# Optimization experiments

Hardware: AMD Instinct MI355X
Metric: run time of the kernel (lower is better)

## Reference

```python
import jax, jax.numpy as jnp
import numpy as np

C_Z = 128
H = 4
D = C_Z // H          # head_dim = 32
BASE = 2 * D // 2     # base_feature_dim = feature_map_multiplier*head_dim//2 = 32
BSZ, S = 1, 256
EPS_LN = 1e-5


def _lin_params(key, fan_in, fan_out):
    kw, kb = jax.random.split(key)
    bound = 1.0 / np.sqrt(fan_in)
    w = jax.random.uniform(kw, (fan_out, fan_in), jnp.float32, -bound, bound)
    b = jax.random.uniform(kb, (fan_out,), jnp.float32, -bound, bound)
    return w, b


def setup_inputs() -> dict:
    key = jax.random.key(0)
    ks = jax.random.split(key, 9)
    z = jax.random.normal(ks[0], (BSZ, S, S, C_Z), jnp.float32)
    pair_mask = jax.random.randint(ks[1], (BSZ, S, S), 0, 2, jnp.int32)
    q_w, q_b = _lin_params(ks[2], C_Z, C_Z)
    k_w, k_b = _lin_params(ks[3], C_Z, C_Z)
    v_w, v_b = _lin_params(ks[4], C_Z, C_Z)
    qf_w, qf_b = _lin_params(ks[5], D, BASE)
    kf_w, kf_b = _lin_params(ks[6], D, BASE)
    g_w, g_b = _lin_params(ks[7], C_Z, C_Z)
    o_w, o_b = _lin_params(ks[8], C_Z, C_Z)
    return {
        'z': z, 'pair_mask': pair_mask,
        'ln_w': jnp.ones((C_Z,), jnp.float32), 'ln_b': jnp.zeros((C_Z,), jnp.float32),
        'q_w': q_w, 'q_b': q_b, 'k_w': k_w, 'k_b': k_b, 'v_w': v_w, 'v_b': v_b,
        'qf_w': qf_w, 'qf_b': qf_b, 'kf_w': kf_w, 'kf_b': kf_b,
        'g_w': g_w, 'g_b': g_b, 'o_w': o_w, 'o_b': o_b,
    }


def _feature_map(t, w, b):
    m = jnp.clip(t @ w.T + b, -8.0, 8.0)
    return jnp.concatenate([jnp.exp(m), jnp.exp(-m)], axis=-1)


def reference(z, pair_mask, ln_w, ln_b, q_w, q_b, k_w, k_b, v_w, v_b,
              qf_w, qf_b, kf_w, kf_b, g_w, g_b, o_w, o_b):
    bsz, seq, _, c = z.shape
    h, d = H, c // H
    mask = pair_mask.astype(z.dtype)                         # [B,S,S]

    # LayerNorm over last dim
    mu = jnp.mean(z, axis=-1, keepdims=True)
    var = jnp.mean(jnp.square(z - mu), axis=-1, keepdims=True)
    zn = (z - mu) * jax.lax.rsqrt(var + EPS_LN) * ln_w + ln_b

    z_rows = zn.reshape(bsz * seq, seq, c)                   # [BS, N, C]
    row_mask = mask.reshape(bsz * seq, seq)[:, None, :, None]  # [BS,1,N,1]

    def proj(w, b):
        return (z_rows @ w.T + b).reshape(bsz * seq, seq, h, d).transpose(0, 2, 1, 3)

    q = proj(q_w, q_b)                                       # [BS,H,N,D]
    k = proj(k_w, k_b)
    v = proj(v_w, v_b) * row_mask

    qf = _feature_map(q, qf_w, qf_b)                         # [BS,H,N,F]
    kf = _feature_map(k, kf_w, kf_b) * row_mask

    kv = jnp.einsum('bhnd,bhne->bhde', kf, v)                # [BS,H,F,D]
    k_sum = kf.sum(axis=-2)                                  # [BS,H,F]
    denom = jnp.maximum(jnp.einsum('bhnd,bhd->bhn', qf, k_sum), 1e-6)
    out = jnp.einsum('bhnd,bhde->bhne', qf, kv) / denom[..., None]

    out = out.transpose(0, 2, 1, 3).reshape(bsz * seq, seq, c)
    gate = jax.nn.sigmoid(z_rows @ g_w.T + g_b)
    out = (gate * out) @ o_w.T + o_b
    out = out.reshape(bsz, seq, seq, c)
    return out * mask[..., None]
```

## Files before the change

kernel.cpp:

```cpp
#include <hip/hip_runtime.h>
#include <stdint.h>

#define DEV __device__ __forceinline__

typedef unsigned short u16;
typedef unsigned int u32;
typedef short bh8 __attribute__((ext_vector_type(8)));
typedef float f32x4 __attribute__((ext_vector_type(4)));

DEV float bf2f(u16 v){ return __uint_as_float(((u32)v)<<16); }
DEV u16 f2bf(float f){
    u32 x = __float_as_uint(f);
    x += 0x7fffu + ((x>>16)&1u);
    return (u16)(x>>16);
}
DEV int2 pk4(float a, float b, float c, float d){
    int2 r;
    r.x = (int)((u32)f2bf(a) | ((u32)f2bf(b)<<16));
    r.y = (int)((u32)f2bf(c) | ((u32)f2bf(d)<<16));
    return r;
}
DEV bh8 ld_frag(const u16* p){
    int4 v = *(const int4*)p;
    union{ int4 i; bh8 h; } u; u.i = v; return u.h;
}
#define MFMA __builtin_amdgcn_mfma_f32_16x16x32_bf16


#define P_LNW 0
#define P_LNB 128
#define P_QW  256
#define P_QB  16640
#define P_KW  16768
#define P_KB  33152
#define P_VW  33280
#define P_VB  49664
#define P_QFW 49792
#define P_QFB 50816
#define P_KFW 50848
#define P_KFB 51872
#define P_GW  51904
#define P_GB  68288
#define P_OW  68416
#define P_OB  84800
#define P_TOT 84928
#define P_CQW 84928
#define P_CQB 101312
#define P_CKW 101440
#define P_CKB 117824

#define NCONV 332

__global__ void prep_params(
    const float* p0, const float* p1, const float* p2, const float* p3,
    const float* p4, const float* p5, const float* p6, const float* p7,
    const float* p8, const float* p9, const float* p10, const float* p11,
    const float* p12, const float* p13, const float* p14, const float* p15,
    u16* __restrict__ dst){
    int b = blockIdx.x, tid = threadIdx.x;
    if(b < NCONV){
        int idx = b*256 + tid;
        if(idx >= P_TOT) return;
        const float* sp = p0; int base = P_LNW;
        if(idx >= P_LNB){ sp = p1;  base = P_LNB; }
        if(idx >= P_QW ){ sp = p2;  base = P_QW;  }
        if(idx >= P_QB ){ sp = p3;  base = P_QB;  }
        if(idx >= P_KW ){ sp = p4;  base = P_KW;  }
        if(idx >= P_KB ){ sp = p5;  base = P_KB;  }
        if(idx >= P_VW ){ sp = p6;  base = P_VW;  }
        if(idx >= P_VB ){ sp = p7;  base = P_VB;  }
        if(idx >= P_QFW){ sp = p8;  base = P_QFW; }
        if(idx >= P_QFB){ sp = p9;  base = P_QFB; }
        if(idx >= P_KFW){ sp = p10; base = P_KFW; }
        if(idx >= P_KFB){ sp = p11; base = P_KFB; }
        if(idx >= P_GW ){ sp = p12; base = P_GW;  }
        if(idx >= P_GB ){ sp = p13; base = P_GB;  }
        if(idx >= P_OW ){ sp = p14; base = P_OW;  }
        if(idx >= P_OB ){ sp = p15; base = P_OB;  }
        dst[idx] = f2bf(sp[idx - base]);
    } else if(b < NCONV + 128){
        int idx = (b - NCONV)*256 + tid;
        int sel = idx >> 14;
        int rem = idx & 16383;
        int h = rem >> 12, j = (rem >> 7) & 31, c = rem & 127;
        const float* FWp = sel ? p10 : p8;
        const float* Wp  = sel ? p4  : p2;
        float s = 0.f;
        #pragma unroll
        for(int d=0; d<32; ++d)
            s += FWp[j*32+d] * Wp[(h*32+d)*128 + c];
        dst[(sel ? P_CKW : P_CQW) + h*4096 + j*128 + c] = f2bf(s);
    } else {
        int t = tid;
        int sel = t >> 7, h = (t >> 5) & 3, j = t & 31;
        const float* FWp = sel ? p10 : p8;
        const float* FBp = sel ? p11 : p9;
        const float* Bp  = sel ? p5  : p3;
        float s = FBp[j];
        #pragma unroll
        for(int d=0; d<32; ++d)
            s += FWp[j*32+d] * Bp[h*32+d];
        dst[(sel ? P_CKB : P_CQB) + h*32 + j] = f2bf(s);
    }
}

__global__ void ln_kernel(const float* __restrict__ zv, const u16* __restrict__ pb,
                          u16* __restrict__ zn){
    int t = blockIdx.x*4 + (threadIdx.x>>6);
    int lane = threadIdx.x & 63;
    float2 v = ((const float2*)zv)[(size_t)t*64 + lane];
    float x0 = v.x, x1 = v.y;
    float s = x0 + x1, s2 = x0*x0 + x1*x1;
    #pragma unroll
    for(int o=1;o<64;o<<=1){ s += __shfl_xor(s,o,64); s2 += __shfl_xor(s2,o,64); }
    float mean = s*(1.f/128.f);
    float var  = s2*(1.f/128.f) - mean*mean;
    float rs = rsqrtf(var + 1e-5f);
    int c0 = 2*lane;
    float w0 = bf2f(pb[P_LNW+c0]), w1 = bf2f(pb[P_LNW+c0+1]);
    float b0 = bf2f(pb[P_LNB+c0]), b1 = bf2f(pb[P_LNB+c0+1]);
    float o0 = (x0-mean)*rs*w0 + b0;
    float o1 = (x1-mean)*rs*w1 + b1;
    u32 po = (u32)f2bf(o0) | ((u32)f2bf(o1)<<16);
    *(u32*)(zn + (size_t)t*128 + c0) = po;
}

#define ST_N 264
#define ST_F 68
#define SM_KF   1024
#define SM_VT   34816
#define SM_QF   1024
#define SM_KVT  51712
#define SM_TOT  56200

__global__ __launch_bounds__(256,2)
void mega_kernel(const u16* __restrict__ zn, const int* __restrict__ mask,
                 const u16* __restrict__ pb, u16* __restrict__ attn){
    __shared__ __align__(16) char smem[SM_TOT];
    float* mask_f = (float*)smem;
    u16* kfT = (u16*)(smem + SM_KF);
    u16* vT  = (u16*)(smem + SM_VT);
    u16* qf  = (u16*)(smem + SM_QF);
    u16* kvT = (u16*)(smem + SM_KVT);

    int g = blockIdx.x, row = g>>2, h = g&3;
    int tid = threadIdx.x, lane = tid & 63, wv = tid >> 6;
    int lm = lane & 15, quad = lane >> 4;

    mask_f[tid] = (float)mask[row*256 + tid];

    bh8 a[4][4];
    {
        const u16* Ab = zn + ((size_t)row*256 + wv*64 + lm)*128 + quad*8;
        #pragma unroll
        for(int mt=0; mt<4; ++mt)
            #pragma unroll
            for(int ks=0; ks<4; ++ks)
                a[mt][ks] = ld_frag(Ab + (size_t)mt*16*128 + ks*32);
    }
    bh8 onesf;
    { union{int4 i; bh8 h;} u; u.i.x=u.i.y=u.i.z=u.i.w=0x3F803F80; onesf = u.h; }

    __syncthreads();

    f32x4 gacc[4][2];
    {
        f32x4 acc[4][6];
        #pragma unroll
        for(int mt=0;mt<4;++mt)
            #pragma unroll
            for(int j=0;j<6;++j) acc[mt][j] = (f32x4){0,0,0,0};
        #pragma unroll
        for(int ks=0; ks<4; ++ks){
            bh8 b[6];
            b[0] = ld_frag(pb + P_CKW + h*4096 + lm*128            + ks*32 + quad*8);
            b[1] = ld_frag(pb + P_CKW + h*4096 + (16+lm)*128       + ks*32 + quad*8);
            b[2] = ld_frag(pb + P_VW + (size_t)(h*32 + lm)*128     + ks*32 + quad*8);
            b[3] = ld_frag(pb + P_VW + (size_t)(h*32 + 16+lm)*128  + ks*32 + quad*8);
            b[4] = ld_frag(pb + P_GW + (size_t)(h*32 + lm)*128     + ks*32 + quad*8);
            b[5] = ld_frag(pb + P_GW + (size_t)(h*32 + 16+lm)*128  + ks*32 + quad*8);
            #pragma unroll
            for(int mt=0; mt<4; ++mt)
                #pragma unroll
                for(int j=0;j<6;++j)
                    acc[mt][j] = MFMA(a[mt][ks], b[j], acc[mt][j], 0,0,0);
        }
        float bk0 = bf2f(pb[P_CKB + h*32 + lm]);
        float bk1 = bf2f(pb[P_CKB + h*32 + 16 + lm]);
        float bv0 = bf2f(pb[P_VB + h*32 + lm]);
        float bv1 = bf2f(pb[P_VB + h*32 + 16 + lm]);
        float bg0 = bf2f(pb[P_GB + h*32 + lm]);
        float bg1 = bf2f(pb[P_GB + h*32 + 16 + lm]);
        #pragma unroll
        for(int mt=0; mt<4; ++mt){
            int n0 = wv*64 + mt*16 + quad*4;
            float ep0[4], em0[4], ep1[4], em1[4], v0[4], v1[4];
            #pragma unroll
            for(int r=0; r<4; ++r){
                float mk = mask_f[n0+r];
                float m0 = fminf(8.f, fmaxf(-8.f, acc[mt][0][r] + bk0));
                float m1 = fminf(8.f, fmaxf(-8.f, acc[mt][1][r] + bk1));
                ep0[r] = __expf( m0)*mk;  em0[r] = __expf(-m0)*mk;
                ep1[r] = __expf( m1)*mk;  em1[r] = __expf(-m1)*mk;
                v0[r] = (acc[mt][2][r] + bv0)*mk;
                v1[r] = (acc[mt][3][r] + bv1)*mk;
                gacc[mt][0][r] = 1.f/(1.f + __expf(-(acc[mt][4][r] + bg0)));
                gacc[mt][1][r] = 1.f/(1.f + __expf(-(acc[mt][5][r] + bg1)));
            }
            *(int2*)(kfT + (size_t)(lm   )*ST_N + n0) = pk4(ep0[0],ep0[1],ep0[2],ep0[3]);
            *(int2*)(kfT + (size_t)(lm+32)*ST_N + n0) = pk4(em0[0],em0[1],em0[2],em0[3]);
            *(int2*)(kfT + (size_t)(lm+16)*ST_N + n0) = pk4(ep1[0],ep1[1],ep1[2],ep1[3]);
            *(int2*)(kfT + (size_t)(lm+48)*ST_N + n0) = pk4(em1[0],em1[1],em1[2],em1[3]);
            *(int2*)(vT  + (size_t)(lm   )*ST_N + n0) = pk4(v0[0],v0[1],v0[2],v0[3]);
            *(int2*)(vT  + (size_t)(16+lm)*ST_N + n0) = pk4(v1[0],v1[1],v1[2],v1[3]);
        }
    }
    __syncthreads();
    {
        f32x4 acc0=(f32x4){0,0,0,0}, acc1=(f32x4){0,0,0,0}, acc2=(f32x4){0,0,0,0};
        #pragma unroll
        for(int ks=0; ks<8; ++ks){
            bh8 aa = ld_frag(kfT + (size_t)(wv*16+lm)*ST_N + ks*32 + quad*8);
            bh8 b0 = ld_frag(vT + (size_t)lm*ST_N      + ks*32 + quad*8);
            bh8 b1 = ld_frag(vT + (size_t)(16+lm)*ST_N + ks*32 + quad*8);
            acc0 = MFMA(aa, b0, acc0, 0,0,0);
            acc1 = MFMA(aa, b1, acc1, 0,0,0);
            acc2 = MFMA(aa, onesf, acc2, 0,0,0);
        }
        int f0 = wv*16 + quad*4;
        *(int2*)(kvT + (size_t)(lm   )*ST_F + f0) = pk4(acc0[0],acc0[1],acc0[2],acc0[3]);
        *(int2*)(kvT + (size_t)(16+lm)*ST_F + f0) = pk4(acc1[0],acc1[1],acc1[2],acc1[3]);
        if(lm==0)
            *(int2*)(kvT + (size_t)32*ST_F + f0) = pk4(acc2[0],acc2[1],acc2[2],acc2[3]);
    }
    __syncthreads();
    {
        f32x4 acc[4][2];
        #pragma unroll
        for(int mt=0;mt<4;++mt){ acc[mt][0]=(f32x4){0,0,0,0}; acc[mt][1]=(f32x4){0,0,0,0}; }
        #pragma unroll
        for(int ks=0; ks<4; ++ks){
            bh8 b0 = ld_frag(pb + P_CQW + h*4096 + lm*128      + ks*32 + quad*8);
            bh8 b1 = ld_frag(pb + P_CQW + h*4096 + (16+lm)*128 + ks*32 + quad*8);
            #pragma unroll
            for(int mt=0; mt<4; ++mt){
                acc[mt][0] = MFMA(a[mt][ks], b0, acc[mt][0], 0,0,0);
                acc[mt][1] = MFMA(a[mt][ks], b1, acc[mt][1], 0,0,0);
            }
        }
        float bb0 = bf2f(pb[P_CQB + h*32 + lm]);
        float bb1 = bf2f(pb[P_CQB + h*32 + 16 + lm]);
        #pragma unroll
        for(int mt=0; mt<4; ++mt)
            #pragma unroll
            for(int r=0; r<4; ++r){
                int n = wv*64 + mt*16 + quad*4 + r;
                float m0 = fminf(8.f, fmaxf(-8.f, acc[mt][0][r] + bb0));
                float m1 = fminf(8.f, fmaxf(-8.f, acc[mt][1][r] + bb1));
                qf[n*ST_F + lm     ] = f2bf(__expf( m0));
                qf[n*ST_F + lm + 32] = f2bf(__expf(-m0));
                qf[n*ST_F + lm + 16] = f2bf(__expf( m1));
                qf[n*ST_F + lm + 48] = f2bf(__expf(-m1));
            }
    }
    __syncthreads();
    {
        f32x4 acc[4][3];
        #pragma unroll
        for(int mt=0;mt<4;++mt)
            #pragma unroll
            for(int nt=0;nt<3;++nt) acc[mt][nt]=(f32x4){0,0,0,0};
        #pragma unroll
        for(int ks=0; ks<2; ++ks){
            bh8 b0 = ld_frag(kvT + (size_t)lm*ST_F      + ks*32 + quad*8);
            bh8 b1 = ld_frag(kvT + (size_t)(16+lm)*ST_F + ks*32 + quad*8);
            bh8 b2 = ld_frag(kvT + (size_t)32*ST_F      + ks*32 + quad*8);
            #pragma unroll
            for(int mt=0; mt<4; ++mt){
                bh8 aa = ld_frag(qf + (size_t)(wv*64+mt*16+lm)*ST_F + ks*32 + quad*8);
                acc[mt][0] = MFMA(aa, b0, acc[mt][0], 0,0,0);
                acc[mt][1] = MFMA(aa, b1, acc[mt][1], 0,0,0);
                acc[mt][2] = MFMA(aa, b2, acc[mt][2], 0,0,0);
            }
        }
        #pragma unroll
        for(int mt=0; mt<4; ++mt)
            #pragma unroll
            for(int r=0; r<4; ++r){
                int n = wv*64 + mt*16 + quad*4 + r;
                float rcp = 1.f / fmaxf(acc[mt][2][r], 1e-6f);
                u16* op = attn + ((size_t)row*256 + n)*128 + h*32;
                op[lm]    = f2bf(acc[mt][0][r]*rcp*gacc[mt][0][r]);
                op[16+lm] = f2bf(acc[mt][1][r]*rcp*gacc[mt][1][r]);
            }
    }
}

__global__ __launch_bounds__(256,2)
void oproj_kernel(const u16* __restrict__ attn, const u16* __restrict__ pb,
                  const int* __restrict__ mask, float* __restrict__ out){
    int tid = threadIdx.x;
    int lane = tid&63, wv = tid>>6;
    int mhalf = (wv>>1)*64, nhalf = (wv&1)*64;
    int lm = lane&15, quad = lane>>4;
    int m0 = blockIdx.x*128;

    f32x4 acc[4][4];
    #pragma unroll
    for(int mt=0;mt<4;++mt)
        #pragma unroll
        for(int nt=0;nt<4;++nt)
            acc[mt][nt] = (f32x4){0.f,0.f,0.f,0.f};

    const u16* Abase = attn + (size_t)(m0 + mhalf + lm)*128 + quad*8;
    const u16* W = pb + P_OW;
    #pragma unroll
    for(int ks=0; ks<4; ++ks){
        bh8 a[4], b[4];
        #pragma unroll
        for(int mt=0; mt<4; ++mt)
            a[mt] = ld_frag(Abase + (size_t)mt*16*128 + ks*32);
        #pragma unroll
        for(int nt=0; nt<4; ++nt)
            b[nt] = ld_frag(W + (size_t)(nhalf + nt*16 + lm)*128 + ks*32 + quad*8);
        #pragma unroll
        for(int mt=0; mt<4; ++mt)
            #pragma unroll
            for(int nt=0; nt<4; ++nt)
                acc[mt][nt] = MFMA(a[mt], b[nt], acc[mt][nt], 0, 0, 0);
    }
    float bv[4];
    #pragma unroll
    for(int nt=0; nt<4; ++nt) bv[nt] = bf2f(pb[P_OB + nhalf + nt*16 + lm]);
    #pragma unroll
    for(int mt=0; mt<4; ++mt){
        int mrow = m0 + mhalf + mt*16 + quad*4;
        float mk[4];
        #pragma unroll
        for(int r=0;r<4;++r) mk[r] = (float)mask[mrow+r];
        #pragma unroll
        for(int r=0; r<4; ++r){
            float* orow = out + (size_t)(mrow + r)*128 + nhalf + lm;
            #pragma unroll
            for(int nt=0; nt<4; ++nt)
                orow[nt*16] = (acc[mt][nt][r] + bv[nt]) * mk[r];
        }
    }
}

extern "C" void kernel_launch(void* const* d_in, const int* in_sizes, int n_in,
                              void* d_out, int out_size, void* d_ws, size_t ws_size,
                              hipStream_t stream){
    const float* z    = (const float*)d_in[0];
    const int*   mask = (const int*)d_in[1];

    char* ws = (char*)d_ws;
    const size_t MB = (size_t)1<<20;
    u16* zn   = (u16*)(ws + 0*MB);
    u16* attn = (u16*)(ws + 16*MB);
    u16* pb   = (u16*)(ws + 32*MB);

    prep_params<<<NCONV+129,256,0,stream>>>(
        (const float*)d_in[2],  (const float*)d_in[3],  (const float*)d_in[4],  (const float*)d_in[5],
        (const float*)d_in[6],  (const float*)d_in[7],  (const float*)d_in[8],  (const float*)d_in[9],
        (const float*)d_in[10], (const float*)d_in[11], (const float*)d_in[12], (const float*)d_in[13],
        (const float*)d_in[14], (const float*)d_in[15], (const float*)d_in[16], (const float*)d_in[17],
        pb);
    ln_kernel<<<16384,256,0,stream>>>(z, pb, zn);
    mega_kernel<<<1024,256,0,stream>>>(zn, mask, pb, attn);
    oproj_kernel<<<512,256,0,stream>>>(attn, pb, mask, (float*)d_out);
}
```

Baseline: 175.8 us.

## Fuse LayerNorm into attention kernel and remap block order across heads

Removes the separate LayerNorm kernel. Each attention block now normalizes its row of z from fp32 directly and stages the bf16 result in XOR-swizzled shared memory before loading MFMA fragments. Block indices are also remapped so that the four head-blocks of one row land far apart in launch order, which spreads them across XCDs while still sharing reads of z through L2. This drops the bf16 zn round trip and one launch, but every row of z is now normalized four times (once per head) and the row loops are serialized with added barriers.

```diff
diff --git a/kernel.cpp b/kernel.cpp
--- a/kernel.cpp
+++ b/kernel.cpp
@@ -104,27 +104,6 @@
     }
 }
 
-__global__ void ln_kernel(const float* __restrict__ zv, const u16* __restrict__ pb,
-                          u16* __restrict__ zn){
-    int t = blockIdx.x*4 + (threadIdx.x>>6);
-    int lane = threadIdx.x & 63;
-    float2 v = ((const float2*)zv)[(size_t)t*64 + lane];
-    float x0 = v.x, x1 = v.y;
-    float s = x0 + x1, s2 = x0*x0 + x1*x1;
-    #pragma unroll
-    for(int o=1;o<64;o<<=1){ s += __shfl_xor(s,o,64); s2 += __shfl_xor(s2,o,64); }
-    float mean = s*(1.f/128.f);
-    float var  = s2*(1.f/128.f) - mean*mean;
-    float rs = rsqrtf(var + 1e-5f);
-    int c0 = 2*lane;
-    float w0 = bf2f(pb[P_LNW+c0]), w1 = bf2f(pb[P_LNW+c0+1]);
-    float b0 = bf2f(pb[P_LNB+c0]), b1 = bf2f(pb[P_LNB+c0+1]);
-    float o0 = (x0-mean)*rs*w0 + b0;
-    float o1 = (x1-mean)*rs*w1 + b1;
-    u32 po = (u32)f2bf(o0) | ((u32)f2bf(o1)<<16);
-    *(u32*)(zn + (size_t)t*128 + c0) = po;
-}
-
 #define ST_N 264
 #define ST_F 68
 #define SM_KF   1024
@@ -134,7 +113,7 @@
 #define SM_TOT  56200
 
 __global__ __launch_bounds__(256,2)
-void mega_kernel(const u16* __restrict__ zn, const int* __restrict__ mask,
+void mega_kernel(const float* __restrict__ z, const int* __restrict__ mask,
                  const u16* __restrict__ pb, u16* __restrict__ attn){
     __shared__ __align__(16) char smem[SM_TOT];
     float* mask_f = (float*)smem;
@@ -143,7 +122,9 @@
     u16* qf  = (u16*)(smem + SM_QF);
     u16* kvT = (u16*)(smem + SM_KVT);
 
-    int g = blockIdx.x, row = g>>2, h = g&3;
+    int g = blockIdx.x;
+    int u = (g & 7)*128 + (g >> 3);
+    int row = u >> 2, h = u & 3;
     int tid = threadIdx.x, lane = tid & 63, wv = tid >> 6;
     int lm = lane & 15, quad = lane >> 4;
 
@@ -151,17 +132,38 @@
 
     bh8 a[4][4];
     {
-        const u16* Ab = zn + ((size_t)row*256 + wv*64 + lm)*128 + quad*8;
-        #pragma unroll
-        for(int mt=0; mt<4; ++mt)
+        char* scr = smem + SM_KF + wv*4096;
+        int c0 = 2*lane;
+        float w0 = bf2f(pb[P_LNW+c0]), w1 = bf2f(pb[P_LNW+c0+1]);
+        float b0 = bf2f(pb[P_LNB+c0]), b1 = bf2f(pb[P_LNB+c0+1]);
+        #pragma unroll 1
+        for(int mt=0; mt<4; ++mt){
+            #pragma unroll 1
+            for(int i=0; i<16; ++i){
+                int t = row*256 + wv*64 + mt*16 + i;
+                float2 v = ((const float2*)z)[(size_t)t*64 + lane];
+                float x0 = v.x, x1 = v.y;
+                float s = x0 + x1, s2 = x0*x0 + x1*x1;
+                #pragma unroll
+                for(int o=1;o<64;o<<=1){ s += __shfl_xor(s,o,64); s2 += __shfl_xor(s2,o,64); }
+                float mean = s*(1.f/128.f);
+                float var  = s2*(1.f/128.f) - mean*mean;
+                float rs = rsqrtf(var + 1e-5f);
+                float o0 = (x0-mean)*rs*w0 + b0;
+                float o1 = (x1-mean)*rs*w1 + b1;
+                u32 po = (u32)f2bf(o0) | ((u32)f2bf(o1)<<16);
+                *(u32*)(scr + ((i*256 + 4*lane) ^ ((i&7)<<4))) = po;
+            }
+            __syncthreads();
             #pragma unroll
             for(int ks=0; ks<4; ++ks)
-                a[mt][ks] = ld_frag(Ab + (size_t)mt*16*128 + ks*32);
+                a[mt][ks] = ld_frag((const u16*)(scr +
+                                ((lm*256 + ks*64 + quad*16) ^ ((lm&7)<<4))));
+            __syncthreads();
+        }
     }
     bh8 onesf;
-    { union{int4 i; bh8 h;} u; u.i.x=u.i.y=u.i.z=u.i.w=0x3F803F80; onesf = u.h; }
-
-    __syncthreads();
+    { union{int4 i; bh8 hh;} u2; u2.i.x=u2.i.y=u2.i.z=u2.i.w=0x3F803F80; onesf = u2.hh; }
 
     f32x4 gacc[4][2];
     {
@@ -356,7 +358,6 @@
 
     char* ws = (char*)d_ws;
     const size_t MB = (size_t)1<<20;
-    u16* zn   = (u16*)(ws + 0*MB);
     u16* attn = (u16*)(ws + 16*MB);
     u16* pb   = (u16*)(ws + 32*MB);
 
@@ -366,7 +367,6 @@
         (const float*)d_in[10], (const float*)d_in[11], (const float*)d_in[12], (const float*)d_in[13],
         (const float*)d_in[14], (const float*)d_in[15], (const float*)d_in[16], (const float*)d_in[17],
         pb);
-    ln_kernel<<<16384,256,0,stream>>>(z, pb, zn);
-    mega_kernel<<<1024,256,0,stream>>>(zn, mask, pb, attn);
+    mega_kernel<<<1024,256,0,stream>>>(z, mask, pb, attn);
     oproj_kernel<<<512,256,0,stream>>>(attn, pb, mask, (float*)d_out);
 }
```

New measurement: 269.9 us. 1.54x slower.

## Use 512 threads per block in mega_kernel and move gate projection to Q phase

Applied to the files above, without the earlier changes.

Doubles the mega_kernel block to 8 waves, each owning 32 rows instead of 64, which halves per-thread register tiles. The kf^T·v reduction is split across feature and d halves, and only half the waves compute the k-sum. The gate projection moves from the K/V phase into the Q phase so fewer accumulators are live at once. The aim is higher occupancy and more latency hiding, at the cost of more waves contending for shared memory and barriers.

```diff
diff --git a/kernel.cpp b/kernel.cpp
--- a/kernel.cpp
+++ b/kernel.cpp
@@ -133,7 +133,7 @@
 #define SM_KVT  51712
 #define SM_TOT  56200
 
-__global__ __launch_bounds__(256,2)
+__global__ __launch_bounds__(512,2)
 void mega_kernel(const u16* __restrict__ zn, const int* __restrict__ mask,
                  const u16* __restrict__ pb, u16* __restrict__ attn){
     __shared__ __align__(16) char smem[SM_TOT];
@@ -147,13 +147,13 @@
     int tid = threadIdx.x, lane = tid & 63, wv = tid >> 6;
     int lm = lane & 15, quad = lane >> 4;
 
-    mask_f[tid] = (float)mask[row*256 + tid];
-
-    bh8 a[4][4];
-    {
-        const u16* Ab = zn + ((size_t)row*256 + wv*64 + lm)*128 + quad*8;
-        #pragma unroll
-        for(int mt=0; mt<4; ++mt)
+    if(tid < 256) mask_f[tid] = (float)mask[row*256 + tid];
+
+    bh8 a[2][4];
+    {
+        const u16* Ab = zn + ((size_t)row*256 + wv*32 + lm)*128 + quad*8;
+        #pragma unroll
+        for(int mt=0; mt<2; ++mt)
             #pragma unroll
             for(int ks=0; ks<4; ++ks)
                 a[mt][ks] = ld_frag(Ab + (size_t)mt*16*128 + ks*32);
@@ -163,37 +163,32 @@
 
     __syncthreads();
 
-    f32x4 gacc[4][2];
-    {
-        f32x4 acc[4][6];
-        #pragma unroll
-        for(int mt=0;mt<4;++mt)
-            #pragma unroll
-            for(int j=0;j<6;++j) acc[mt][j] = (f32x4){0,0,0,0};
+    {
+        f32x4 acc[2][4];
+        #pragma unroll
+        for(int mt=0;mt<2;++mt)
+            #pragma unroll
+            for(int j=0;j<4;++j) acc[mt][j] = (f32x4){0,0,0,0};
         #pragma unroll
         for(int ks=0; ks<4; ++ks){
-            bh8 b[6];
+            bh8 b[4];
             b[0] = ld_frag(pb + P_CKW + h*4096 + lm*128            + ks*32 + quad*8);
             b[1] = ld_frag(pb + P_CKW + h*4096 + (16+lm)*128       + ks*32 + quad*8);
             b[2] = ld_frag(pb + P_VW + (size_t)(h*32 + lm)*128     + ks*32 + quad*8);
             b[3] = ld_frag(pb + P_VW + (size_t)(h*32 + 16+lm)*128  + ks*32 + quad*8);
-            b[4] = ld_frag(pb + P_GW + (size_t)(h*32 + lm)*128     + ks*32 + quad*8);
-            b[5] = ld_frag(pb + P_GW + (size_t)(h*32 + 16+lm)*128  + ks*32 + quad*8);
-            #pragma unroll
-            for(int mt=0; mt<4; ++mt)
+            #pragma unroll
+            for(int mt=0; mt<2; ++mt)
                 #pragma unroll
-                for(int j=0;j<6;++j)
+                for(int j=0;j<4;++j)
                     acc[mt][j] = MFMA(a[mt][ks], b[j], acc[mt][j], 0,0,0);
         }
         float bk0 = bf2f(pb[P_CKB + h*32 + lm]);
         float bk1 = bf2f(pb[P_CKB + h*32 + 16 + lm]);
         float bv0 = bf2f(pb[P_VB + h*32 + lm]);
         float bv1 = bf2f(pb[P_VB + h*32 + 16 + lm]);
-        float bg0 = bf2f(pb[P_GB + h*32 + lm]);
-        float bg1 = bf2f(pb[P_GB + h*32 + 16 + lm]);
-        #pragma unroll
-        for(int mt=0; mt<4; ++mt){
-            int n0 = wv*64 + mt*16 + quad*4;
+        #pragma unroll
+        for(int mt=0; mt<2; ++mt){
+            int n0 = wv*32 + mt*16 + quad*4;
             float ep0[4], em0[4], ep1[4], em1[4], v0[4], v1[4];
             #pragma unroll
             for(int r=0; r<4; ++r){
@@ -204,8 +199,6 @@
                 ep1[r] = __expf( m1)*mk;  em1[r] = __expf(-m1)*mk;
                 v0[r] = (acc[mt][2][r] + bv0)*mk;
                 v1[r] = (acc[mt][3][r] + bv1)*mk;
-                gacc[mt][0][r] = 1.f/(1.f + __expf(-(acc[mt][4][r] + bg0)));
-                gacc[mt][1][r] = 1.f/(1.f + __expf(-(acc[mt][5][r] + bg1)));
             }
             *(int2*)(kfT + (size_t)(lm   )*ST_N + n0) = pk4(ep0[0],ep0[1],ep0[2],ep0[3]);
             *(int2*)(kfT + (size_t)(lm+32)*ST_N + n0) = pk4(em0[0],em0[1],em0[2],em0[3]);
@@ -217,57 +210,66 @@
     }
     __syncthreads();
     {
-        f32x4 acc0=(f32x4){0,0,0,0}, acc1=(f32x4){0,0,0,0}, acc2=(f32x4){0,0,0,0};
+        int fw = wv >> 1, dw = wv & 1;
+        f32x4 acc0=(f32x4){0,0,0,0}, acc2=(f32x4){0,0,0,0};
         #pragma unroll
         for(int ks=0; ks<8; ++ks){
-            bh8 aa = ld_frag(kfT + (size_t)(wv*16+lm)*ST_N + ks*32 + quad*8);
-            bh8 b0 = ld_frag(vT + (size_t)lm*ST_N      + ks*32 + quad*8);
-            bh8 b1 = ld_frag(vT + (size_t)(16+lm)*ST_N + ks*32 + quad*8);
+            bh8 aa = ld_frag(kfT + (size_t)(fw*16+lm)*ST_N + ks*32 + quad*8);
+            bh8 b0 = ld_frag(vT + (size_t)(dw*16+lm)*ST_N + ks*32 + quad*8);
             acc0 = MFMA(aa, b0, acc0, 0,0,0);
-            acc1 = MFMA(aa, b1, acc1, 0,0,0);
-            acc2 = MFMA(aa, onesf, acc2, 0,0,0);
-        }
-        int f0 = wv*16 + quad*4;
-        *(int2*)(kvT + (size_t)(lm   )*ST_F + f0) = pk4(acc0[0],acc0[1],acc0[2],acc0[3]);
-        *(int2*)(kvT + (size_t)(16+lm)*ST_F + f0) = pk4(acc1[0],acc1[1],acc1[2],acc1[3]);
-        if(lm==0)
+            if(dw == 0)
+                acc2 = MFMA(aa, onesf, acc2, 0,0,0);
+        }
+        int f0 = fw*16 + quad*4;
+        *(int2*)(kvT + (size_t)(dw*16+lm)*ST_F + f0) = pk4(acc0[0],acc0[1],acc0[2],acc0[3]);
+        if(dw==0 && lm==0)
             *(int2*)(kvT + (size_t)32*ST_F + f0) = pk4(acc2[0],acc2[1],acc2[2],acc2[3]);
     }
     __syncthreads();
-    {
-        f32x4 acc[4][2];
-        #pragma unroll
-        for(int mt=0;mt<4;++mt){ acc[mt][0]=(f32x4){0,0,0,0}; acc[mt][1]=(f32x4){0,0,0,0}; }
+    f32x4 gacc[2][2];
+    {
+        f32x4 acc[2][4];
+        #pragma unroll
+        for(int mt=0;mt<2;++mt)
+            #pragma unroll
+            for(int j=0;j<4;++j) acc[mt][j] = (f32x4){0,0,0,0};
         #pragma unroll
         for(int ks=0; ks<4; ++ks){
-            bh8 b0 = ld_frag(pb + P_CQW + h*4096 + lm*128      + ks*32 + quad*8);
-            bh8 b1 = ld_frag(pb + P_CQW + h*4096 + (16+lm)*128 + ks*32 + quad*8);
-            #pragma unroll
-            for(int mt=0; mt<4; ++mt){
-                acc[mt][0] = MFMA(a[mt][ks], b0, acc[mt][0], 0,0,0);
-                acc[mt][1] = MFMA(a[mt][ks], b1, acc[mt][1], 0,0,0);
-            }
+            bh8 b[4];
+            b[0] = ld_frag(pb + P_CQW + h*4096 + lm*128            + ks*32 + quad*8);
+            b[1] = ld_frag(pb + P_CQW + h*4096 + (16+lm)*128       + ks*32 + quad*8);
+            b[2] = ld_frag(pb + P_GW + (size_t)(h*32 + lm)*128     + ks*32 + quad*8);
+            b[3] = ld_frag(pb + P_GW + (size_t)(h*32 + 16+lm)*128  + ks*32 + quad*8);
+            #pragma unroll
+            for(int mt=0; mt<2; ++mt)
+                #pragma unroll
+                for(int j=0;j<4;++j)
+                    acc[mt][j] = MFMA(a[mt][ks], b[j], acc[mt][j], 0,0,0);
         }
         float bb0 = bf2f(pb[P_CQB + h*32 + lm]);
         float bb1 = bf2f(pb[P_CQB + h*32 + 16 + lm]);
-        #pragma unroll
-        for(int mt=0; mt<4; ++mt)
+        float bg0 = bf2f(pb[P_GB + h*32 + lm]);
+        float bg1 = bf2f(pb[P_GB + h*32 + 16 + lm]);
+        #pragma unroll
+        for(int mt=0; mt<2; ++mt)
             #pragma unroll
             for(int r=0; r<4; ++r){
-                int n = wv*64 + mt*16 + quad*4 + r;
+                int n = wv*32 + mt*16 + quad*4 + r;
                 float m0 = fminf(8.f, fmaxf(-8.f, acc[mt][0][r] + bb0));
                 float m1 = fminf(8.f, fmaxf(-8.f, acc[mt][1][r] + bb1));
                 qf[n*ST_F + lm     ] = f2bf(__expf( m0));
                 qf[n*ST_F + lm + 32] = f2bf(__expf(-m0));
                 qf[n*ST_F + lm + 16] = f2bf(__expf( m1));
                 qf[n*ST_F + lm + 48] = f2bf(__expf(-m1));
+                gacc[mt][0][r] = 1.f/(1.f + __expf(-(acc[mt][2][r] + bg0)));
+                gacc[mt][1][r] = 1.f/(1.f + __expf(-(acc[mt][3][r] + bg1)));
             }
     }
     __syncthreads();
     {
-        f32x4 acc[4][3];
-        #pragma unroll
-        for(int mt=0;mt<4;++mt)
+        f32x4 acc[2][3];
+        #pragma unroll
+        for(int mt=0;mt<2;++mt)
             #pragma unroll
             for(int nt=0;nt<3;++nt) acc[mt][nt]=(f32x4){0,0,0,0};
         #pragma unroll
@@ -276,18 +278,18 @@
             bh8 b1 = ld_frag(kvT + (size_t)(16+lm)*ST_F + ks*32 + quad*8);
             bh8 b2 = ld_frag(kvT + (size_t)32*ST_F      + ks*32 + quad*8);
             #pragma unroll
-            for(int mt=0; mt<4; ++mt){
-                bh8 aa = ld_frag(qf + (size_t)(wv*64+mt*16+lm)*ST_F + ks*32 + quad*8);
+            for(int mt=0; mt<2; ++mt){
+                bh8 aa = ld_frag(qf + (size_t)(wv*32+mt*16+lm)*ST_F + ks*32 + quad*8);
                 acc[mt][0] = MFMA(aa, b0, acc[mt][0], 0,0,0);
                 acc[mt][1] = MFMA(aa, b1, acc[mt][1], 0,0,0);
                 acc[mt][2] = MFMA(aa, b2, acc[mt][2], 0,0,0);
             }
         }
         #pragma unroll
-        for(int mt=0; mt<4; ++mt)
+        for(int mt=0; mt<2; ++mt)
             #pragma unroll
             for(int r=0; r<4; ++r){
-                int n = wv*64 + mt*16 + quad*4 + r;
+                int n = wv*32 + mt*16 + quad*4 + r;
                 float rcp = 1.f / fmaxf(acc[mt][2][r], 1e-6f);
                 u16* op = attn + ((size_t)row*256 + n)*128 + h*32;
                 op[lm]    = f2bf(acc[mt][0][r]*rcp*gacc[mt][0][r]);
@@ -367,6 +369,6 @@
         (const float*)d_in[14], (const float*)d_in[15], (const float*)d_in[16], (const float*)d_in[17],
         pb);
     ln_kernel<<<16384,256,0,stream>>>(z, pb, zn);
-    mega_kernel<<<1024,256,0,stream>>>(zn, mask, pb, attn);
+    mega_kernel<<<1024,512,0,stream>>>(zn, mask, pb, attn);
     oproj_kernel<<<512,256,0,stream>>>(attn, pb, mask, (float*)d_out);
 }
```

New measurement: 186.5 us. 1.06x slower.
